# Kernel tuning notes

Measured on AMD Instinct MI355X. Metric: run time of the kernel, lower is better.

The kernel has to match this reference:

```python
import jax, jax.numpy as jnp
import numpy as np

B = 2
SEQ = 384            # args.seq_len (per-stock sub-sequence length)
N_AUX = 4            # len(args.aux_tickers)
S = SEQ * N_AUX + 1  # global separator token + tiled sub-sequences
D_MODEL = 512
NHEAD = 8
HEAD_DIM = 64
ROPE = 32            # qk_rope_dim
KV_C = 256
Q_C = 384
D_FF = 1536
H2 = NHEAD * 2       # differential attention sub-heads
DH = HEAD_DIM // 2
RH = ROPE // 2
EPS = 1.1920929e-07  # torch RMSNorm default eps (fp32 machine eps)
SCALING = 1.0 / ((HEAD_DIM + ROPE) // 2)
LAMBDA_INIT = 0.8 - 0.6 * float(np.exp(-0.3 * 0))  # depth=0 -> 0.2


def rmsnorm(x, w, eps=EPS):
    return x * jax.lax.rsqrt(jnp.mean(jnp.square(x), -1, keepdims=True) + eps) * w


def apply_rope(xs, cos, sin):
    # xs: [B, N_AUX, SEQ, H2, RH]; cos/sin: [SEQ, RH//2]
    xr = xs[..., 0::2]
    xi = xs[..., 1::2]
    c = cos[None, None, :, None, :]
    s = sin[None, None, :, None, :]
    yr = xr * c - xi * s
    yi = xr * s + xi * c
    return jnp.stack([yr, yi], axis=-1).reshape(xs.shape)


def _build_mask():
    causal = np.triu(np.ones((SEQ, SEQ), np.bool_), 1)
    tiled = np.tile(causal, (N_AUX, N_AUX))
    m = np.ones((S, S), np.bool_)
    m[:, 0] = False          # everyone attends to global separator
    m[1:, 1:] = tiled
    return jnp.asarray(m)[None, None]  # [1,1,S,S], True = masked


MASK = _build_mask()


def setup_inputs() -> dict:
    key = jax.random.key(0)
    ks = jax.random.split(key, 16)

    def w(k, shape, std=0.02):
        return jax.random.normal(k, shape, jnp.float32) * std

    x = jax.random.normal(ks[0], (B, S, D_MODEL), jnp.float32)
    # rope table: complex [SEQ, ROPE//4] stored as (cos, sin)
    pairs = ROPE // 4
    inv = 1.0 / (10000.0 ** (np.arange(pairs, dtype=np.float64) / pairs))
    ang = np.outer(np.arange(SEQ), inv)
    freqs = jnp.asarray(np.stack([np.cos(ang), np.sin(ang)], -1), jnp.float32)
    return {
        'x': x,
        'freqs': freqs,
        'W_kv_down': w(ks[1], (D_MODEL, KV_C + ROPE)),
        'W_q_down': w(ks[2], (D_MODEL, Q_C)),
        'W_kv_up': w(ks[3], (KV_C, NHEAD * HEAD_DIM * 2)),
        'W_q_up': w(ks[4], (Q_C, NHEAD * (HEAD_DIM + ROPE))),
        'kv_norm_w': jnp.ones((KV_C,), jnp.float32),
        'q_norm_w': jnp.ones((Q_C,), jnp.float32),
        'W_o': w(ks[5], (NHEAD * HEAD_DIM, D_MODEL)),
        'lambda_q1': w(ks[6], (DH,), 0.1),
        'lambda_k1': w(ks[7], (DH,), 0.1),
        'lambda_q2': w(ks[8], (DH,), 0.1),
        'lambda_k2': w(ks[9], (DH,), 0.1),
        'head_norm_w': jnp.ones((HEAD_DIM,), jnp.float32),
        'norm1_w': jnp.ones((D_MODEL,), jnp.float32),
        'norm2_w': jnp.ones((D_MODEL,), jnp.float32),
        'W_ff_in': w(ks[10], (D_MODEL, 2 * D_FF)),
        'W_ff_out': w(ks[11], (D_FF, D_MODEL)),
    }


def reference(x, freqs, W_kv_down, W_q_down, W_kv_up, W_q_up, kv_norm_w, q_norm_w,
              W_o, lambda_q1, lambda_k1, lambda_q2, lambda_k2, head_norm_w,
              norm1_w, norm2_w, W_ff_in, W_ff_out):
    cos, sin = freqs[..., 0], freqs[..., 1]
    # ---- attention block (pre-norm) ----
    h = rmsnorm(x, norm1_w)
    ckv_full = h @ W_kv_down                               # [B,S,KV_C+ROPE]
    c_kv, k_rope = ckv_full[..., :KV_C], ckv_full[..., KV_C:]
    kv = (rmsnorm(c_kv, kv_norm_w) @ W_kv_up).reshape(B, S, NHEAD, 2 * HEAD_DIM)
    k, v = kv[..., :HEAD_DIM], kv[..., HEAD_DIM:]
    k = k.reshape(B, S, H2, DH)
    qf = (rmsnorm(h @ W_q_down, q_norm_w) @ W_q_up).reshape(B, S, NHEAD, HEAD_DIM + ROPE)
    q, q_rope = qf[..., :HEAD_DIM], qf[..., HEAD_DIM:]
    q = q.reshape(B, S, H2, DH)
    k_rope = jnp.broadcast_to(k_rope[:, :, None, :], (B, S, NHEAD, ROPE)).reshape(B, S, H2, RH)
    q_rope = q_rope.reshape(B, S, H2, RH)
    # split off global separator token, rope per sub-sequence
    q_sep, q_rot = q_rope[:, :1], q_rope[:, 1:].reshape(B, N_AUX, SEQ, H2, RH)
    k_sep, k_rot = k_rope[:, :1], k_rope[:, 1:].reshape(B, N_AUX, SEQ, H2, RH)
    q_rot = apply_rope(q_rot, cos, sin).reshape(B, S - 1, H2, RH)
    k_rot = apply_rope(k_rot, cos, sin).reshape(B, S - 1, H2, RH)
    q_rope = jnp.concatenate([q_sep, q_rot], axis=1)
    k_rope = jnp.concatenate([k_sep, k_rot], axis=1)
    qh = jnp.concatenate([q, q_rope], -1).transpose(0, 2, 1, 3)  # [B,H2,S,DH+RH]
    kh = jnp.concatenate([k, k_rope], -1).transpose(0, 2, 1, 3)
    a = jnp.einsum('bhqd,bhkd->bhqk', qh, kh) * SCALING
    abs_a = jnp.where(MASK, -1e9, jnp.abs(a))
    p = jnp.sign(a) * jax.nn.softmax(abs_a, axis=-1)
    lam = (jnp.exp(jnp.sum(lambda_q1 * lambda_k1)) -
           jnp.exp(jnp.sum(lambda_q2 * lambda_k2)) + LAMBDA_INIT)
    p = p.reshape(B, NHEAD, 2, S, S)
    G = jnp.mean(p[:, :, 0], axis=-1, keepdims=True)
    att = p[:, :, 0] - lam * p[:, :, 1] + G * lam
    att = jnp.where(MASK, 0.0, att)
    o = jnp.einsum('bhqk,bkhd->bqhd', att, v)              # [B,S,NHEAD,HEAD_DIM]
    o = rmsnorm(o, head_norm_w, 1e-5).reshape(B, S, NHEAD * HEAD_DIM)
    x = x + o @ W_o
    # ---- SwiGLU FFN ----
    h2 = rmsnorm(x, norm2_w)
    uv = h2 @ W_ff_in
    u, g = uv[..., :D_FF], uv[..., D_FF:]
    return x + (u * jax.nn.silu(g)) @ W_ff_out
```

## Files before the change

### kernel.cpp

```cpp
#include <hip/hip_runtime.h>

#define NB 2
#define SEQN 384
#define NS 1537
#define NS_PAD 1600
#define NH 8
#define H2N 16
#define NM (NB*NS)
#define DFF 1536
#define EPS1 1.1920929e-07f
#define SCAL (1.0f/48.0f)
#define SC2 (SCAL * 1.4426950408889634f)

typedef __bf16 bf16x8 __attribute__((ext_vector_type(8)));
typedef _Float16 f16x8 __attribute__((ext_vector_type(8)));
typedef float f32x4 __attribute__((ext_vector_type(4)));

__device__ __forceinline__ unsigned short f2bf(float f) {
    unsigned int u = __builtin_bit_cast(unsigned int, f);
    u += 0x7FFFu + ((u >> 16) & 1u);
    return (unsigned short)(u >> 16);
}
__device__ __forceinline__ float bf2f(unsigned short h) {
    unsigned int u = ((unsigned int)h) << 16;
    return __builtin_bit_cast(float, u);
}

__global__ void transpose_split(const float* __restrict__ w, unsigned short* __restrict__ hi,
                                unsigned short* __restrict__ lo, int K, int N) {
    __shared__ float tile[32][33];
    int k0 = blockIdx.x * 32, n0 = blockIdx.y * 32;
    int tx = threadIdx.x & 31, ty4 = (threadIdx.x >> 5) * 4;
    for (int i = 0; i < 4; i++) {
        int k = k0 + ty4 + i, n = n0 + tx;
        tile[ty4 + i][tx] = (k < K && n < N) ? w[(size_t)k * N + n] : 0.f;
    }
    __syncthreads();
    for (int i = 0; i < 4; i++) {
        int n = n0 + ty4 + i, k = k0 + tx;
        if (n < N && k < K) {
            float v = tile[tx][ty4 + i];
            unsigned short hb = f2bf(v);
            size_t o = (size_t)n * K + k;
            hi[o] = hb;
            if (lo) lo[o] = f2bf(v - bf2f(hb));
        }
    }
}

__global__ void lam_kernel(const float* q1, const float* k1, const float* q2, const float* k2,
                           float* out) {
    int t = threadIdx.x;
    float p1 = 0.f, p2 = 0.f;
    if (t < 32) { p1 = q1[t] * k1[t]; p2 = q2[t] * k2[t]; }
    for (int o = 1; o < 32; o <<= 1) { p1 += __shfl_xor(p1, o); p2 += __shfl_xor(p2, o); }
    if (t == 0) out[0] = expf(p1) - expf(p2) + 0.2f;
}

__global__ __launch_bounds__(256) void rmsnorm_k(const float* __restrict__ in,
    const float* __restrict__ w, unsigned short* __restrict__ hi, unsigned short* __restrict__ lo,
    int in_stride, int C, float eps) {
    int row = blockIdx.x;
    const float* x = in + (size_t)row * in_stride;
    float ss = 0.f;
    for (int j = threadIdx.x; j < C; j += 256) { float v = x[j]; ss += v * v; }
    for (int o = 1; o < 64; o <<= 1) ss += __shfl_xor(ss, o);
    __shared__ float red[4];
    if ((threadIdx.x & 63) == 0) red[threadIdx.x >> 6] = ss;
    __syncthreads();
    ss = red[0] + red[1] + red[2] + red[3];
    float rs = rsqrtf(ss / (float)C + eps);
    for (int j = threadIdx.x; j < C; j += 256) {
        float y = x[j] * rs * w[j];
        unsigned short hb = f2bf(y);
        hi[(size_t)row * C + j] = hb;
        if (lo) lo[(size_t)row * C + j] = f2bf(y - bf2f(hb));
    }
}

__global__ __launch_bounds__(256) void gemm_single(const unsigned short* __restrict__ A,
    const unsigned short* __restrict__ Bt, float* __restrict__ C_, const float* __restrict__ res,
    int M, int N, int K) {
    __shared__ unsigned short As[128][32];
    __shared__ unsigned short Bs[64][32];
    int m0 = blockIdx.x * 128, n0 = blockIdx.y * 64;
    int tid = threadIdx.x;
    int lane = tid & 63, wid = tid >> 6;
    int wr = wid >> 1, wc = wid & 1;
    int r = lane & 15, g = lane >> 4;
    int lrow = tid >> 2, lk = (tid & 3) * 8;
    f32x4 acc[4][2] = {};
    int ar0 = m0 + lrow, ar1 = m0 + 64 + lrow, brow = n0 + lrow;
    bool a0ok = ar0 < M, a1ok = ar1 < M, bok = brow < N;
    size_t a0off = (size_t)ar0 * K + lk, a1off = (size_t)ar1 * K + lk, boff = (size_t)brow * K + lk;
    for (int k0 = 0; k0 < K; k0 += 32) {
        uint4 av0 = {0,0,0,0}, av1 = {0,0,0,0}, bv = {0,0,0,0};
        if (a0ok) av0 = *(const uint4*)(A + a0off + k0);
        if (a1ok) av1 = *(const uint4*)(A + a1off + k0);
        if (bok)  bv  = *(const uint4*)(Bt + boff + k0);
        __syncthreads();
        *(uint4*)&As[lrow][lk] = av0;
        *(uint4*)&As[64 + lrow][lk] = av1;
        *(uint4*)&Bs[lrow][lk] = bv;
        __syncthreads();
        bf16x8 a[4], bb[2];
        #pragma unroll
        for (int i = 0; i < 4; i++) a[i] = *(const bf16x8*)&As[wr * 64 + i * 16 + r][g * 8];
        #pragma unroll
        for (int j = 0; j < 2; j++) bb[j] = *(const bf16x8*)&Bs[wc * 32 + j * 16 + r][g * 8];
        #pragma unroll
        for (int i = 0; i < 4; i++)
            #pragma unroll
            for (int j = 0; j < 2; j++)
                acc[i][j] = __builtin_amdgcn_mfma_f32_16x16x32_bf16(a[i], bb[j], acc[i][j], 0, 0, 0);
    }
    #pragma unroll
    for (int i = 0; i < 4; i++)
        #pragma unroll
        for (int j = 0; j < 2; j++) {
            int col = n0 + wc * 32 + j * 16 + r;
            if (col >= N) continue;
            #pragma unroll
            for (int e = 0; e < 4; e++) {
                int row = m0 + wr * 64 + i * 16 + g * 4 + e;
                if (row >= M) continue;
                float v = acc[i][j][e];
                if (res) v += res[(size_t)row * N + col];
                C_[(size_t)row * N + col] = v;
            }
        }
}

__global__ __launch_bounds__(256) void gemm_x3(const unsigned short* __restrict__ Ah,
    const unsigned short* __restrict__ Al, const unsigned short* __restrict__ Bh,
    const unsigned short* __restrict__ Bl, float* __restrict__ C_, int M, int N, int K) {
    __shared__ unsigned short AsH[128][32], AsL[128][32], BsH[64][32], BsL[64][32];
    int m0 = blockIdx.x * 128, n0 = blockIdx.y * 64;
    int tid = threadIdx.x;
    int lane = tid & 63, wid = tid >> 6;
    int wr = wid >> 1, wc = wid & 1;
    int r = lane & 15, g = lane >> 4;
    int lrow = tid >> 2, lk = (tid & 3) * 8;
    f32x4 acc[4][2] = {};
    int ar0 = m0 + lrow, ar1 = m0 + 64 + lrow, brow = n0 + lrow;
    bool a0ok = ar0 < M, a1ok = ar1 < M, bok = brow < N;
    size_t a0off = (size_t)ar0 * K + lk, a1off = (size_t)ar1 * K + lk, boff = (size_t)brow * K + lk;
    for (int k0 = 0; k0 < K; k0 += 32) {
        uint4 ah0 = {0,0,0,0}, al0 = {0,0,0,0}, ah1 = {0,0,0,0}, al1 = {0,0,0,0};
        uint4 bh0 = {0,0,0,0}, bl0 = {0,0,0,0};
        if (a0ok) { ah0 = *(const uint4*)(Ah + a0off + k0); al0 = *(const uint4*)(Al + a0off + k0); }
        if (a1ok) { ah1 = *(const uint4*)(Ah + a1off + k0); al1 = *(const uint4*)(Al + a1off + k0); }
        if (bok)  { bh0 = *(const uint4*)(Bh + boff + k0);  bl0 = *(const uint4*)(Bl + boff + k0); }
        __syncthreads();
        *(uint4*)&AsH[lrow][lk] = ah0; *(uint4*)&AsH[64 + lrow][lk] = ah1;
        *(uint4*)&AsL[lrow][lk] = al0; *(uint4*)&AsL[64 + lrow][lk] = al1;
        *(uint4*)&BsH[lrow][lk] = bh0; *(uint4*)&BsL[lrow][lk] = bl0;
        __syncthreads();
        bf16x8 ah[4], al[4], bh[2], bl[2];
        #pragma unroll
        for (int i = 0; i < 4; i++) {
            ah[i] = *(const bf16x8*)&AsH[wr * 64 + i * 16 + r][g * 8];
            al[i] = *(const bf16x8*)&AsL[wr * 64 + i * 16 + r][g * 8];
        }
        #pragma unroll
        for (int j = 0; j < 2; j++) {
            bh[j] = *(const bf16x8*)&BsH[wc * 32 + j * 16 + r][g * 8];
            bl[j] = *(const bf16x8*)&BsL[wc * 32 + j * 16 + r][g * 8];
        }
        #pragma unroll
        for (int i = 0; i < 4; i++)
            #pragma unroll
            for (int j = 0; j < 2; j++) {
                acc[i][j] = __builtin_amdgcn_mfma_f32_16x16x32_bf16(al[i], bh[j], acc[i][j], 0, 0, 0);
                acc[i][j] = __builtin_amdgcn_mfma_f32_16x16x32_bf16(ah[i], bl[j], acc[i][j], 0, 0, 0);
                acc[i][j] = __builtin_amdgcn_mfma_f32_16x16x32_bf16(ah[i], bh[j], acc[i][j], 0, 0, 0);
            }
    }
    #pragma unroll
    for (int i = 0; i < 4; i++)
        #pragma unroll
        for (int j = 0; j < 2; j++) {
            int col = n0 + wc * 32 + j * 16 + r;
            if (col >= N) continue;
            #pragma unroll
            for (int e = 0; e < 4; e++) {
                int row = m0 + wr * 64 + i * 16 + g * 4 + e;
                if (row < M) C_[(size_t)row * N + col] = acc[i][j][e];
            }
        }
}

__global__ void assemble2(const float* __restrict__ qf_, const float* __restrict__ kvf,
    const float* __restrict__ ckv, const float* __restrict__ freqs,
    _Float16* __restrict__ qgh, _Float16* __restrict__ qgl,
    _Float16* __restrict__ kgh, _Float16* __restrict__ kgl) {
    size_t idx = (size_t)blockIdx.x * 256 + threadIdx.x;
    const size_t total = (size_t)NB * H2N * NS_PAD * 32;
    if (idx >= total) return;
    int j2 = (int)(idx & 31);
    size_t t = idx >> 5;
    int s = (int)(t % NS_PAD); size_t r = t / NS_PAD;
    int sub = (int)(r & 1); r >>= 1;
    int h = (int)(r & 7); int b = (int)(r >> 3);
    float2 qv = make_float2(0.f, 0.f), kv2 = make_float2(0.f, 0.f);
    if (s < NS && j2 < 24) {
        size_t bs = (size_t)b * NS + s;
        if (j2 < 16) {
            const float* qp = qf_ + bs * 768 + h * 96 + sub * 32 + j2 * 2;
            qv = make_float2(qp[0], qp[1]);
            const float* kp = kvf + bs * 1024 + h * 128 + sub * 32 + j2 * 2;
            kv2 = make_float2(kp[0], kp[1]);
        } else {
            int i = j2 - 16;
            const float* qp = qf_ + bs * 768 + h * 96 + 64 + sub * 16 + 2 * i;
            float xr = qp[0], xi = qp[1];
            const float* kp = ckv + bs * 288 + 256 + sub * 16 + 2 * i;
            float yr = kp[0], yi = kp[1];
            if (s == 0) {
                qv = make_float2(xr, xi);
                kv2 = make_float2(yr, yi);
            } else {
                int pos = (s - 1) % SEQN;
                float c = freqs[pos * 16 + 2 * i], sn = freqs[pos * 16 + 2 * i + 1];
                qv = make_float2(xr * c - xi * sn, xr * sn + xi * c);
                kv2 = make_float2(yr * c - yi * sn, yr * sn + yi * c);
            }
        }
    }
    _Float16 qx = (_Float16)qv.x, qy = (_Float16)qv.y;
    _Float16 kx = (_Float16)kv2.x, ky = (_Float16)kv2.y;
    qgh[idx * 2] = qx; qgh[idx * 2 + 1] = qy;
    kgh[idx * 2] = kx; kgh[idx * 2 + 1] = ky;
    qgl[idx * 2] = (_Float16)(qv.x - (float)qx); qgl[idx * 2 + 1] = (_Float16)(qv.y - (float)qy);
    kgl[idx * 2] = (_Float16)(kv2.x - (float)kx); kgl[idx * 2 + 1] = (_Float16)(kv2.y - (float)ky);
}

__global__ __launch_bounds__(256) void vtrans(const float* __restrict__ kvf,
                                              _Float16* __restrict__ vt) {
    __shared__ float tile[64][65];
    int k0 = blockIdx.x * 64;
    int b = blockIdx.y >> 3, h = blockIdx.y & 7;
    int tid = threadIdx.x;
    int row = tid >> 2, cq = (tid & 3) * 16;
    for (int i = 0; i < 16; i++) {
        int key = k0 + row;
        tile[row][cq + i] = (key < NS)
            ? kvf[((size_t)(b * NS + key)) * 1024 + h * 128 + 64 + cq + i] : 0.f;
    }
    __syncthreads();
    int d = tid >> 2, kq = (tid & 3) * 16;
    for (int i = 0; i < 16; i++)
        vt[((size_t)((b * 8 + h) * 64 + d)) * NS_PAD + k0 + kq + i] = (_Float16)tile[kq + i][d];
}

__global__ __launch_bounds__(256) void sum4_k(const float* __restrict__ kvf,
                                              float* __restrict__ S4) {
    int bh = blockIdx.x; int b = bh >> 3, h = bh & 7;
    int p0 = blockIdx.y * 64;
    int t = threadIdx.x;
    int d = t & 63, psub = t >> 6;
    for (int i = 0; i < 16; i++) {
        int p = p0 + psub + i * 4;
        float s = 0.f;
        #pragma unroll
        for (int c = 0; c < 4; c++)
            s += kvf[((size_t)(b * NS + 1 + c * SEQN + p)) * 1024 + h * 128 + 64 + d];
        S4[((size_t)bh * SEQN + p) * 64 + d] = s;
    }
}

__global__ void prefix_k(const float* __restrict__ S4, float* __restrict__ P4) {
    int bh = blockIdx.x; int d = threadIdx.x;
    float acc = 0.f;
    for (int p = 0; p < SEQN; p++) {
        acc += S4[((size_t)bh * SEQN + p) * 64 + d];
        P4[((size_t)bh * SEQN + p) * 64 + d] = acc;
    }
}

__global__ __launch_bounds__(256) void flash_attn(
    const _Float16* __restrict__ qgh, const _Float16* __restrict__ qgl,
    const _Float16* __restrict__ kgh, const _Float16* __restrict__ kgl,
    const _Float16* __restrict__ vt,
    const float* __restrict__ kvf, const float* __restrict__ P4,
    const float* __restrict__ lamp, const float* __restrict__ hw,
    unsigned short* __restrict__ o_n) {
    __shared__ _Float16 Ksh[2][64][72];
    __shared__ _Float16 Ksl[2][64][72];
    __shared__ _Float16 Vt[64][72];
    __shared__ _Float16 Pl[4][16][72];
    const int tile = blockIdx.x, h = blockIdx.y, b = blockIdx.z;
    const int qs0 = tile * 64;
    const int tid = threadIdx.x;
    const int wave = tid >> 6, lane = tid & 63;
    const int r = lane & 15, g = lane >> 4;
    const int qrow = qs0 + wave * 16;
    const size_t sh0 = (size_t)((b * 8 + h) * 2);

    f16x8 qfh[2][2], qfl[2][2];
    #pragma unroll
    for (int sub = 0; sub < 2; sub++)
        #pragma unroll
        for (int ks = 0; ks < 2; ks++) {
            size_t off = ((sh0 + sub) * NS_PAD + qrow + r) * 64 + ks * 32 + g * 8;
            qfh[sub][ks] = *(const f16x8*)(qgh + off);
            qfl[sub][ks] = *(const f16x8*)(qgl + off);
        }

    float z0p[4] = {0.f,0.f,0.f,0.f}, g0p[4] = {0.f,0.f,0.f,0.f}, z1p[4] = {0.f,0.f,0.f,0.f};
    f32x4 O0[4], O1[4];
    #pragma unroll
    for (int e = 0; e < 4; e++) { O0[e] = (f32x4){0.f,0.f,0.f,0.f}; O1[e] = (f32x4){0.f,0.f,0.f,0.f}; }
    int qpos[4];
    #pragma unroll
    for (int e = 0; e < 4; e++) {
        int q = qrow + g * 4 + e;
        qpos[e] = (q == 0) ? -1 : (q - 1) % SEQN;
    }
    int lo = qs0 < 1 ? 1 : qs0;
    int hi = qs0 + 63 < NS - 1 ? qs0 + 63 : NS - 1;
    int maxpos = ((lo - 1) / SEQN != (hi - 1) / SEQN) ? (SEQN - 1) : (hi - 1) % SEQN;

    for (int c = 0; c < 4; c++) {
        int nb = (c == 0) ? ((maxpos + 2 + 63) >> 6) : ((maxpos + 1 + 63) >> 6);
        int kstart = (c == 0) ? 0 : (c * SEQN + 1);
        int cbase = c * SEQN + 1;
        for (int j = 0; j < nb; j++) {
            int kbase = kstart + j * 64;
            __syncthreads();
            #pragma unroll
            for (int i = 0; i < 4; i++) {
                int chunk = i * 256 + tid;
                int arr = chunk >> 9;
                int cc = chunk & 511;
                int row = cc >> 3, c8 = (cc & 7) * 8;
                size_t goff = ((sh0 + arr) * NS_PAD + kbase + row) * 64 + c8;
                *(uint4*)&Ksh[arr][row][c8] = *(const uint4*)(kgh + goff);
                *(uint4*)&Ksl[arr][row][c8] = *(const uint4*)(kgl + goff);
            }
            #pragma unroll
            for (int i = 0; i < 2; i++) {
                int cc = i * 256 + tid;
                int d = cc >> 3, c8 = (cc & 7) * 8;
                *(uint4*)&Vt[d][c8] =
                    *(const uint4*)(vt + ((size_t)((b * 8 + h) * 64 + d)) * NS_PAD + kbase + c8);
            }
            __syncthreads();

            f16x8 bv[4][2];
            #pragma unroll
            for (int dt = 0; dt < 4; dt++)
                #pragma unroll
                for (int ks = 0; ks < 2; ks++)
                    bv[dt][ks] = *(const f16x8*)&Vt[dt * 16 + r][ks * 32 + g * 8];

            bool um[4][4];
            #pragma unroll
            for (int t4 = 0; t4 < 4; t4++) {
                int kk2 = kbase + t4 * 16 + r;
                int rel = kk2 - cbase;
                #pragma unroll
                for (int e = 0; e < 4; e++)
                    um[e][t4] = (kk2 == 0) ||
                                ((unsigned)rel < (unsigned)SEQN && rel <= qpos[e]);
            }

            #pragma unroll
            for (int sub = 0; sub < 2; sub++) {
                f32x4 acc[4];
                #pragma unroll
                for (int t4 = 0; t4 < 4; t4++) acc[t4] = (f32x4){0.f,0.f,0.f,0.f};
                #pragma unroll
                for (int t4 = 0; t4 < 4; t4++)
                    #pragma unroll
                    for (int ks = 0; ks < 2; ks++) {
                        f16x8 bkh = *(const f16x8*)&Ksh[sub][t4 * 16 + r][ks * 32 + g * 8];
                        f16x8 bkl = *(const f16x8*)&Ksl[sub][t4 * 16 + r][ks * 32 + g * 8];
                        acc[t4] = __builtin_amdgcn_mfma_f32_16x16x32_f16(qfl[sub][ks], bkh, acc[t4], 0, 0, 0);
                        acc[t4] = __builtin_amdgcn_mfma_f32_16x16x32_f16(qfh[sub][ks], bkl, acc[t4], 0, 0, 0);
                        acc[t4] = __builtin_amdgcn_mfma_f32_16x16x32_f16(qfh[sub][ks], bkh, acc[t4], 0, 0, 0);
                    }
                #pragma unroll
                for (int e = 0; e < 4; e++) {
                    #pragma unroll
                    for (int t4 = 0; t4 < 4; t4++) {
                        float a = acc[t4][e];
                        float ef = exp2f(fabsf(a) * SC2);
                        float ev = um[e][t4] ? ef : 0.f;
                        float pvv = copysignf(ev, a);
                        if (sub == 0) { z0p[e] += ev; g0p[e] += pvv; }
                        else          { z1p[e] += ev; }
                        Pl[wave][g * 4 + e][t4 * 16 + r] = (_Float16)pvv;
                    }
                }
                __builtin_amdgcn_wave_barrier();
                f16x8 pa0 = *(const f16x8*)&Pl[wave][r][g * 8];
                f16x8 pa1 = *(const f16x8*)&Pl[wave][r][32 + g * 8];
                #pragma unroll
                for (int dt = 0; dt < 4; dt++) {
                    if (sub == 0) {
                        O0[dt] = __builtin_amdgcn_mfma_f32_16x16x32_f16(pa0, bv[dt][0], O0[dt], 0, 0, 0);
                        O0[dt] = __builtin_amdgcn_mfma_f32_16x16x32_f16(pa1, bv[dt][1], O0[dt], 0, 0, 0);
                    } else {
                        O1[dt] = __builtin_amdgcn_mfma_f32_16x16x32_f16(pa0, bv[dt][0], O1[dt], 0, 0, 0);
                        O1[dt] = __builtin_amdgcn_mfma_f32_16x16x32_f16(pa1, bv[dt][1], O1[dt], 0, 0, 0);
                    }
                }
            }
        }
    }

    float lam = lamp[0];
    float v0d[4], hwd[4];
    #pragma unroll
    for (int dt = 0; dt < 4; dt++) {
        int d = dt * 16 + r;
        v0d[dt] = kvf[((size_t)(b * NS)) * 1024 + h * 128 + 64 + d];
        hwd[dt] = hw[d];
    }
    #pragma unroll
    for (int e = 0; e < 4; e++) {
        float z0 = z0p[e], g0 = g0p[e], z1 = z1p[e];
        #pragma unroll
        for (int o = 1; o < 16; o <<= 1) {
            z0 += __shfl_xor(z0, o); g0 += __shfl_xor(g0, o); z1 += __shfl_xor(z1, o);
        }
        int q = qrow + g * 4 + e;
        if (q >= NS) continue;
        float iz0 = 1.f / z0;
        float l1 = lam / z1;
        float Gl = lam * g0 * iz0 * (1.f / (float)NS);
        float of[4]; float ss = 0.f;
        #pragma unroll
        for (int dt = 0; dt < 4; dt++) {
            float vs = v0d[dt];
            if (qpos[e] >= 0)
                vs += P4[((size_t)(b * 8 + h) * SEQN + qpos[e]) * 64 + dt * 16 + r];
            float o = O0[dt][e] * iz0 - O1[dt][e] * l1 + Gl * vs;
            of[dt] = o; ss += o * o;
        }
        ss += __shfl_xor(ss, 1); ss += __shfl_xor(ss, 2);
        ss += __shfl_xor(ss, 4); ss += __shfl_xor(ss, 8);
        float rs = rsqrtf(ss / 64.f + 1e-5f);
        #pragma unroll
        for (int dt = 0; dt < 4; dt++)
            o_n[((size_t)(b * NS + q)) * 512 + h * 64 + dt * 16 + r] = f2bf(of[dt] * rs * hwd[dt]);
    }
}

__global__ void swiglu_k(const float* __restrict__ uv, unsigned short* __restrict__ act) {
    size_t idx = (size_t)blockIdx.x * 256 + threadIdx.x;
    if (idx >= (size_t)NM * DFF) return;
    size_t mrow = idx / DFF; int j = (int)(idx % DFF);
    float u = uv[mrow * (2 * DFF) + j];
    float gg = uv[mrow * (2 * DFF) + DFF + j];
    float sg = gg / (1.f + __expf(-gg));
    act[idx] = f2bf(u * sg);
}

extern "C" void kernel_launch(void* const* d_in, const int* in_sizes, int n_in,
                              void* d_out, int out_size, void* d_ws, size_t ws_size,
                              hipStream_t stream) {
    (void)in_sizes; (void)n_in; (void)out_size; (void)ws_size;
    const float* x    = (const float*)d_in[0];
    const float* freqs= (const float*)d_in[1];
    const float* Wkvd = (const float*)d_in[2];
    const float* Wqd  = (const float*)d_in[3];
    const float* Wkvu = (const float*)d_in[4];
    const float* Wqu  = (const float*)d_in[5];
    const float* kvnw = (const float*)d_in[6];
    const float* qnw  = (const float*)d_in[7];
    const float* Wo   = (const float*)d_in[8];
    const float* lq1  = (const float*)d_in[9];
    const float* lk1  = (const float*)d_in[10];
    const float* lq2  = (const float*)d_in[11];
    const float* lk2  = (const float*)d_in[12];
    const float* hnw  = (const float*)d_in[13];
    const float* n1w  = (const float*)d_in[14];
    const float* n2w  = (const float*)d_in[15];
    const float* Wffi = (const float*)d_in[16];
    const float* Wffo = (const float*)d_in[17];
    float* out = (float*)d_out;

    char* p = (char*)d_ws;
    auto alloc = [&](size_t nbytes) -> char* {
        char* r = p; p += (nbytes + 255) & ~(size_t)255; return r;
    };
    unsigned short* wkvd_h = (unsigned short*)alloc((size_t)512 * 288 * 2);
    unsigned short* wkvd_l = (unsigned short*)alloc((size_t)512 * 288 * 2);
    unsigned short* wqd_h  = (unsigned short*)alloc((size_t)512 * 384 * 2);
    unsigned short* wqd_l  = (unsigned short*)alloc((size_t)512 * 384 * 2);
    unsigned short* wkvu_h = (unsigned short*)alloc((size_t)256 * 1024 * 2);
    unsigned short* wkvu_l = (unsigned short*)alloc((size_t)256 * 1024 * 2);
    unsigned short* wqu_h  = (unsigned short*)alloc((size_t)384 * 768 * 2);
    unsigned short* wqu_l  = (unsigned short*)alloc((size_t)384 * 768 * 2);
    unsigned short* wo_h   = (unsigned short*)alloc((size_t)512 * 512 * 2);
    unsigned short* wffi_h = (unsigned short*)alloc((size_t)512 * 3072 * 2);
    unsigned short* wffo_h = (unsigned short*)alloc((size_t)1536 * 512 * 2);
    unsigned short* h_hi   = (unsigned short*)alloc((size_t)NM * 512 * 2);
    unsigned short* h_lo   = (unsigned short*)alloc((size_t)NM * 512 * 2);
    char* cq0 = p;
    float* ckv = (float*)alloc((size_t)NM * 288 * 4);
    float* qd  = (float*)alloc((size_t)NM * 384 * 4);
    float* x2  = (float*)cq0;
    char* nb0 = p;
    unsigned short* ckvn_h = (unsigned short*)alloc((size_t)NM * 256 * 2);
    unsigned short* ckvn_l = (unsigned short*)alloc((size_t)NM * 256 * 2);
    unsigned short* qdn_h  = (unsigned short*)alloc((size_t)NM * 384 * 2);
    unsigned short* qdn_l  = (unsigned short*)alloc((size_t)NM * 384 * 2);
    unsigned short* o_n    = (unsigned short*)alloc((size_t)NM * 512 * 2);
    unsigned short* h2     = (unsigned short*)alloc((size_t)NM * 512 * 2);
    unsigned short* act    = (unsigned short*)nb0;
    char* r0 = p;
    float* kvf = (float*)alloc((size_t)NM * 1024 * 4);
    float* qff = (float*)alloc((size_t)NM * 768 * 4);
    _Float16* qgh = (_Float16*)alloc((size_t)NB * H2N * NS_PAD * 64 * 2);
    _Float16* qgl = (_Float16*)alloc((size_t)NB * H2N * NS_PAD * 64 * 2);
    _Float16* kgh = (_Float16*)alloc((size_t)NB * H2N * NS_PAD * 64 * 2);
    _Float16* kgl = (_Float16*)alloc((size_t)NB * H2N * NS_PAD * 64 * 2);
    _Float16* vt  = (_Float16*)alloc((size_t)NB * NH * 64 * NS_PAD * 2);
    float* P4     = (float*)alloc((size_t)NB * NH * SEQN * 64 * 4);
    float* S4     = (float*)alloc((size_t)NB * NH * SEQN * 64 * 4);
    float* uv     = (float*)r0;
    float* lamv   = (float*)alloc(256);

    auto T = [&](const float* w, unsigned short* hi_, unsigned short* lo_, int K, int N) {
        dim3 g((K + 31) / 32, (N + 31) / 32);
        transpose_split<<<g, 256, 0, stream>>>(w, hi_, lo_, K, N);
    };
    T(Wkvd, wkvd_h, wkvd_l, 512, 288);
    T(Wqd,  wqd_h,  wqd_l,  512, 384);
    T(Wkvu, wkvu_h, wkvu_l, 256, 1024);
    T(Wqu,  wqu_h,  wqu_l,  384, 768);
    T(Wo,   wo_h,   nullptr, 512, 512);
    T(Wffi, wffi_h, nullptr, 512, 3072);
    T(Wffo, wffo_h, nullptr, 1536, 512);
    lam_kernel<<<1, 64, 0, stream>>>(lq1, lk1, lq2, lk2, lamv);

    rmsnorm_k<<<NM, 256, 0, stream>>>(x, n1w, h_hi, h_lo, 512, 512, EPS1);

    const int GX = (NM + 127) / 128;
    gemm_x3<<<dim3(GX, (288 + 63) / 64), 256, 0, stream>>>(h_hi, h_lo, wkvd_h, wkvd_l, ckv, NM, 288, 512);
    gemm_x3<<<dim3(GX, (384 + 63) / 64), 256, 0, stream>>>(h_hi, h_lo, wqd_h, wqd_l, qd, NM, 384, 512);

    rmsnorm_k<<<NM, 256, 0, stream>>>(ckv, kvnw, ckvn_h, ckvn_l, 288, 256, EPS1);
    rmsnorm_k<<<NM, 256, 0, stream>>>(qd, qnw, qdn_h, qdn_l, 384, 384, EPS1);

    gemm_x3<<<dim3(GX, 1024 / 64), 256, 0, stream>>>(ckvn_h, ckvn_l, wkvu_h, wkvu_l, kvf, NM, 1024, 256);
    gemm_x3<<<dim3(GX, 768 / 64), 256, 0, stream>>>(qdn_h, qdn_l, wqu_h, wqu_l, qff, NM, 768, 384);

    {
        size_t total = (size_t)NB * H2N * NS_PAD * 32;
        assemble2<<<dim3((unsigned)((total + 255) / 256)), 256, 0, stream>>>(
            qff, kvf, ckv, freqs, qgh, qgl, kgh, kgl);
    }
    vtrans<<<dim3(NS_PAD / 64, NB * NH), 256, 0, stream>>>(kvf, vt);
    sum4_k<<<dim3(NB * NH, SEQN / 64), 256, 0, stream>>>(kvf, S4);
    prefix_k<<<dim3(NB * NH), 64, 0, stream>>>(S4, P4);

    flash_attn<<<dim3((NS + 63) / 64, NH, NB), 256, 0, stream>>>(
        qgh, qgl, kgh, kgl, vt, kvf, P4, lamv, hnw, o_n);

    gemm_single<<<dim3(GX, 512 / 64), 256, 0, stream>>>(o_n, wo_h, x2, x, NM, 512, 512);
    rmsnorm_k<<<NM, 256, 0, stream>>>(x2, n2w, h2, nullptr, 512, 512, EPS1);
    gemm_single<<<dim3(GX, 3072 / 64), 256, 0, stream>>>(h2, wffi_h, uv, nullptr, NM, 3072, 512);
    {
        size_t total = (size_t)NM * DFF;
        swiglu_k<<<dim3((unsigned)((total + 255) / 256)), 256, 0, stream>>>(uv, act);
    }
    gemm_single<<<dim3(GX, 512 / 64), 256, 0, stream>>>(act, wffo_h, out, x2, NM, 512, 1536);
}
```

Before: 331.0 us.

## Split attention across key chunks, merge weight transposes, fuse prefix sum

```diff
diff --git a/kernel.cpp b/kernel.cpp
--- a/kernel.cpp
+++ b/kernel.cpp
@@ -26,20 +26,32 @@
     return __builtin_bit_cast(float, u);
 }
 
-__global__ void transpose_split(const float* __restrict__ w, unsigned short* __restrict__ hi,
-                                unsigned short* __restrict__ lo, int K, int N) {
+struct TD { const float* w; unsigned short* hi; unsigned short* lo; int K; int N; };
+struct TD7 { TD d[7]; int tend[7]; };
+
+__global__ __launch_bounds__(256) void transpose_all(TD7 a) {
     __shared__ float tile[32][33];
-    int k0 = blockIdx.x * 32, n0 = blockIdx.y * 32;
+    int t = blockIdx.x;
+    int i = 0;
+    while (t >= a.tend[i]) i++;
+    int base = (i == 0) ? 0 : a.tend[i - 1];
+    int lt = t - base;
+    const float* w = a.d[i].w;
+    unsigned short* hi = a.d[i].hi;
+    unsigned short* lo = a.d[i].lo;
+    int K = a.d[i].K, N = a.d[i].N;
+    int kt = (K + 31) / 32;
+    int k0 = (lt % kt) * 32, n0 = (lt / kt) * 32;
     int tx = threadIdx.x & 31, ty4 = (threadIdx.x >> 5) * 4;
-    for (int i = 0; i < 4; i++) {
-        int k = k0 + ty4 + i, n = n0 + tx;
-        tile[ty4 + i][tx] = (k < K && n < N) ? w[(size_t)k * N + n] : 0.f;
+    for (int q = 0; q < 4; q++) {
+        int k = k0 + ty4 + q, n = n0 + tx;
+        tile[ty4 + q][tx] = (k < K && n < N) ? w[(size_t)k * N + n] : 0.f;
     }
     __syncthreads();
-    for (int i = 0; i < 4; i++) {
-        int n = n0 + ty4 + i, k = k0 + tx;
+    for (int q = 0; q < 4; q++) {
+        int n = n0 + ty4 + q, k = k0 + tx;
         if (n < N && k < K) {
-            float v = tile[tx][ty4 + i];
+            float v = tile[tx][ty4 + q];
             unsigned short hb = f2bf(v);
             size_t o = (size_t)n * K + k;
             hi[o] = hb;
@@ -253,49 +265,51 @@
         vt[((size_t)((b * 8 + h) * 64 + d)) * NS_PAD + k0 + kq + i] = (_Float16)tile[kq + i][d];
 }
 
-__global__ __launch_bounds__(256) void sum4_k(const float* __restrict__ kvf,
-                                              float* __restrict__ S4) {
+__global__ __launch_bounds__(256) void prefix2_k(const float* __restrict__ kvf,
+                                                 float* __restrict__ P4) {
+    __shared__ float tot[4][64];
     int bh = blockIdx.x; int b = bh >> 3, h = bh & 7;
-    int p0 = blockIdx.y * 64;
-    int t = threadIdx.x;
-    int d = t & 63, psub = t >> 6;
-    for (int i = 0; i < 16; i++) {
-        int p = p0 + psub + i * 4;
+    int d = threadIdx.x & 63, ps = threadIdx.x >> 6;
+    int p0 = ps * 96;
+    float run = 0.f;
+    for (int i = 0; i < 96; i++) {
+        int p = p0 + i;
         float s = 0.f;
         #pragma unroll
         for (int c = 0; c < 4; c++)
             s += kvf[((size_t)(b * NS + 1 + c * SEQN + p)) * 1024 + h * 128 + 64 + d];
-        S4[((size_t)bh * SEQN + p) * 64 + d] = s;
-    }
-}
-
-__global__ void prefix_k(const float* __restrict__ S4, float* __restrict__ P4) {
-    int bh = blockIdx.x; int d = threadIdx.x;
-    float acc = 0.f;
-    for (int p = 0; p < SEQN; p++) {
-        acc += S4[((size_t)bh * SEQN + p) * 64 + d];
-        P4[((size_t)bh * SEQN + p) * 64 + d] = acc;
-    }
-}
-
-__global__ __launch_bounds__(256) void flash_attn(
+        run += s;
+        P4[((size_t)bh * SEQN + p) * 64 + d] = run;
+    }
+    tot[ps][d] = run;
+    __syncthreads();
+    if (ps > 0) {
+        float off = 0.f;
+        for (int j = 0; j < ps; j++) off += tot[j][d];
+        for (int i = 0; i < 96; i++)
+            P4[((size_t)bh * SEQN + p0 + i) * 64 + d] += off;
+    }
+}
+
+__global__ __launch_bounds__(256) void flash_split(
     const _Float16* __restrict__ qgh, const _Float16* __restrict__ qgl,
     const _Float16* __restrict__ kgh, const _Float16* __restrict__ kgl,
     const _Float16* __restrict__ vt,
-    const float* __restrict__ kvf, const float* __restrict__ P4,
-    const float* __restrict__ lamp, const float* __restrict__ hw,
-    unsigned short* __restrict__ o_n) {
+    float* __restrict__ Opart, float* __restrict__ zpart) {
     __shared__ _Float16 Ksh[2][64][72];
     __shared__ _Float16 Ksl[2][64][72];
     __shared__ _Float16 Vt[64][72];
     __shared__ _Float16 Pl[4][16][72];
-    const int tile = blockIdx.x, h = blockIdx.y, b = blockIdx.z;
+    const int tile = blockIdx.x;
+    const int h = blockIdx.y & 7, split = blockIdx.y >> 3;
+    const int b = blockIdx.z;
+    const int bh = b * 8 + h;
     const int qs0 = tile * 64;
     const int tid = threadIdx.x;
     const int wave = tid >> 6, lane = tid & 63;
     const int r = lane & 15, g = lane >> 4;
     const int qrow = qs0 + wave * 16;
-    const size_t sh0 = (size_t)((b * 8 + h) * 2);
+    const size_t sh0 = (size_t)(bh * 2);
 
     f16x8 qfh[2][2], qfl[2][2];
     #pragma unroll
@@ -321,7 +335,7 @@
     int hi = qs0 + 63 < NS - 1 ? qs0 + 63 : NS - 1;
     int maxpos = ((lo - 1) / SEQN != (hi - 1) / SEQN) ? (SEQN - 1) : (hi - 1) % SEQN;
 
-    for (int c = 0; c < 4; c++) {
+    for (int c = 2 * split; c < 2 * split + 2; c++) {
         int nb = (c == 0) ? ((maxpos + 2 + 63) >> 6) : ((maxpos + 1 + 63) >> 6);
         int kstart = (c == 0) ? 0 : (c * SEQN + 1);
         int cbase = c * SEQN + 1;
@@ -343,7 +357,7 @@
                 int cc = i * 256 + tid;
                 int d = cc >> 3, c8 = (cc & 7) * 8;
                 *(uint4*)&Vt[d][c8] =
-                    *(const uint4*)(vt + ((size_t)((b * 8 + h) * 64 + d)) * NS_PAD + kbase + c8);
+                    *(const uint4*)(vt + ((size_t)(bh * 64 + d)) * NS_PAD + kbase + c8);
             }
             __syncthreads();
 
@@ -410,14 +424,6 @@
         }
     }
 
-    float lam = lamp[0];
-    float v0d[4], hwd[4];
-    #pragma unroll
-    for (int dt = 0; dt < 4; dt++) {
-        int d = dt * 16 + r;
-        v0d[dt] = kvf[((size_t)(b * NS)) * 1024 + h * 128 + 64 + d];
-        hwd[dt] = hw[d];
-    }
     #pragma unroll
     for (int e = 0; e < 4; e++) {
         float z0 = z0p[e], g0 = g0p[e], z1 = z1p[e];
@@ -426,25 +432,66 @@
             z0 += __shfl_xor(z0, o); g0 += __shfl_xor(g0, o); z1 += __shfl_xor(z1, o);
         }
         int q = qrow + g * 4 + e;
-        if (q >= NS) continue;
-        float iz0 = 1.f / z0;
-        float l1 = lam / z1;
-        float Gl = lam * g0 * iz0 * (1.f / (float)NS);
-        float of[4]; float ss = 0.f;
-        #pragma unroll
-        for (int dt = 0; dt < 4; dt++) {
-            float vs = v0d[dt];
-            if (qpos[e] >= 0)
-                vs += P4[((size_t)(b * 8 + h) * SEQN + qpos[e]) * 64 + dt * 16 + r];
-            float o = O0[dt][e] * iz0 - O1[dt][e] * l1 + Gl * vs;
-            of[dt] = o; ss += o * o;
-        }
-        ss += __shfl_xor(ss, 1); ss += __shfl_xor(ss, 2);
-        ss += __shfl_xor(ss, 4); ss += __shfl_xor(ss, 8);
-        float rs = rsqrtf(ss / 64.f + 1e-5f);
-        #pragma unroll
-        for (int dt = 0; dt < 4; dt++)
-            o_n[((size_t)(b * NS + q)) * 512 + h * 64 + dt * 16 + r] = f2bf(of[dt] * rs * hwd[dt]);
+        if (q < NS) {
+            if (r == 0) {
+                float* zp = zpart + (((size_t)split * 16 + bh) * NS + q) * 4;
+                zp[0] = z0; zp[1] = g0; zp[2] = z1;
+            }
+            float* op = Opart + (((size_t)split * 16 + bh) * NS + q) * 128;
+            #pragma unroll
+            for (int dt = 0; dt < 4; dt++) {
+                op[dt * 16 + r] = O0[dt][e];
+                op[64 + dt * 16 + r] = O1[dt][e];
+            }
+        }
+    }
+}
+
+__global__ __launch_bounds__(256) void combine_attn(const float* __restrict__ Opart,
+    const float* __restrict__ zpart, const float* __restrict__ kvf,
+    const float* __restrict__ P4, const float* __restrict__ lamp,
+    const float* __restrict__ hw, unsigned short* __restrict__ o_n) {
+    int b = blockIdx.z, h = blockIdx.y, bh = b * 8 + h;
+    int ql = threadIdx.x >> 2, dp = threadIdx.x & 3;
+    int q = blockIdx.x * 64 + ql;
+    bool ok = q < NS;
+    int qc = ok ? q : 0;
+    float lam = lamp[0];
+    size_t i0 = ((size_t)0 * 16 + bh) * NS + qc;
+    size_t i1 = ((size_t)1 * 16 + bh) * NS + qc;
+    const float* za = zpart + i0 * 4;
+    const float* zb = zpart + i1 * 4;
+    float z0 = za[0] + zb[0], g0 = za[1] + zb[1], z1 = za[2] + zb[2];
+    float iz0 = 1.f / z0;
+    float l1 = lam / z1;
+    float Gl = lam * g0 * iz0 * (1.f / (float)NS);
+    int qpos = (q == 0) ? -1 : (q - 1) % SEQN;
+    const float* oa = Opart + i0 * 128 + dp * 16;
+    const float* ob = Opart + i1 * 128 + dp * 16;
+    float of[16]; float ss = 0.f;
+    #pragma unroll
+    for (int i = 0; i < 16; i++) {
+        int d = dp * 16 + i;
+        float O0 = oa[i] + ob[i];
+        float O1 = oa[64 + i] + ob[64 + i];
+        float vs = kvf[((size_t)(b * NS)) * 1024 + h * 128 + 64 + d];
+        if (qpos >= 0) vs += P4[((size_t)bh * SEQN + qpos) * 64 + d];
+        float o = O0 * iz0 - O1 * l1 + Gl * vs;
+        of[i] = o; ss += o * o;
+    }
+    ss += __shfl_xor(ss, 1); ss += __shfl_xor(ss, 2);
+    float rs = rsqrtf(ss / 64.f + 1e-5f);
+    if (ok) {
+        unsigned int pk[8];
+        #pragma unroll
+        for (int i = 0; i < 8; i++) {
+            unsigned int a = f2bf(of[2 * i] * rs * hw[dp * 16 + 2 * i]);
+            unsigned int c = f2bf(of[2 * i + 1] * rs * hw[dp * 16 + 2 * i + 1]);
+            pk[i] = a | (c << 16);
+        }
+        unsigned short* dst = o_n + ((size_t)(b * NS + q)) * 512 + h * 64 + dp * 16;
+        *(uint4*)dst = *(uint4*)&pk[0];
+        *(uint4*)(dst + 8) = *(uint4*)&pk[4];
     }
 }
 
@@ -520,21 +567,26 @@
     _Float16* kgl = (_Float16*)alloc((size_t)NB * H2N * NS_PAD * 64 * 2);
     _Float16* vt  = (_Float16*)alloc((size_t)NB * NH * 64 * NS_PAD * 2);
     float* P4     = (float*)alloc((size_t)NB * NH * SEQN * 64 * 4);
-    float* S4     = (float*)alloc((size_t)NB * NH * SEQN * 64 * 4);
+    float* Opart  = (float*)alloc((size_t)2 * 16 * NS * 128 * 4);
+    float* zpart  = (float*)alloc((size_t)2 * 16 * NS * 4 * 4);
     float* uv     = (float*)r0;
     float* lamv   = (float*)alloc(256);
 
-    auto T = [&](const float* w, unsigned short* hi_, unsigned short* lo_, int K, int N) {
-        dim3 g((K + 31) / 32, (N + 31) / 32);
-        transpose_split<<<g, 256, 0, stream>>>(w, hi_, lo_, K, N);
-    };
-    T(Wkvd, wkvd_h, wkvd_l, 512, 288);
-    T(Wqd,  wqd_h,  wqd_l,  512, 384);
-    T(Wkvu, wkvu_h, wkvu_l, 256, 1024);
-    T(Wqu,  wqu_h,  wqu_l,  384, 768);
-    T(Wo,   wo_h,   nullptr, 512, 512);
-    T(Wffi, wffi_h, nullptr, 512, 3072);
-    T(Wffo, wffo_h, nullptr, 1536, 512);
+    {
+        TD7 a;
+        const float* ws_[7] = {Wkvd, Wqd, Wkvu, Wqu, Wo, Wffi, Wffo};
+        unsigned short* his[7] = {wkvd_h, wqd_h, wkvu_h, wqu_h, wo_h, wffi_h, wffo_h};
+        unsigned short* los[7] = {wkvd_l, wqd_l, wkvu_l, wqu_l, nullptr, nullptr, nullptr};
+        int Ks[7] = {512, 512, 256, 384, 512, 512, 1536};
+        int Ns[7] = {288, 384, 1024, 768, 512, 3072, 512};
+        int cum = 0;
+        for (int i = 0; i < 7; i++) {
+            a.d[i] = TD{ws_[i], his[i], los[i], Ks[i], Ns[i]};
+            cum += ((Ks[i] + 31) / 32) * ((Ns[i] + 31) / 32);
+            a.tend[i] = cum;
+        }
+        transpose_all<<<dim3(cum), 256, 0, stream>>>(a);
+    }
     lam_kernel<<<1, 64, 0, stream>>>(lq1, lk1, lq2, lk2, lamv);
 
     rmsnorm_k<<<NM, 256, 0, stream>>>(x, n1w, h_hi, h_lo, 512, 512, EPS1);
@@ -555,11 +607,12 @@
             qff, kvf, ckv, freqs, qgh, qgl, kgh, kgl);
     }
     vtrans<<<dim3(NS_PAD / 64, NB * NH), 256, 0, stream>>>(kvf, vt);
-    sum4_k<<<dim3(NB * NH, SEQN / 64), 256, 0, stream>>>(kvf, S4);
-    prefix_k<<<dim3(NB * NH), 64, 0, stream>>>(S4, P4);
-
-    flash_attn<<<dim3((NS + 63) / 64, NH, NB), 256, 0, stream>>>(
-        qgh, qgl, kgh, kgl, vt, kvf, P4, lamv, hnw, o_n);
+    prefix2_k<<<dim3(NB * NH), 256, 0, stream>>>(kvf, P4);
+
+    flash_split<<<dim3((NS + 63) / 64, 16, NB), 256, 0, stream>>>(
+        qgh, qgl, kgh, kgl, vt, Opart, zpart);
+    combine_attn<<<dim3((NS + 63) / 64, NH, NB), 256, 0, stream>>>(
+        Opart, zpart, kvf, P4, lamv, hnw, o_n);
 
     gemm_single<<<dim3(GX, 512 / 64), 256, 0, stream>>>(o_n, wo_h, x2, x, NM, 512, 512);
     rmsnorm_k<<<NM, 256, 0, stream>>>(x2, n2w, h2, nullptr, 512, 512, EPS1);
```

Result: no change. 333.2 us (+0.7%).
